# Optimization experiments

Measured on AMD Instinct MI355X. Metric: run time of the kernel, lower is better.

The kernel has to match this reference:

```python
import jax, jax.numpy as jnp
import numpy as np

DIM = 576
SCALE = DIM ** -0.5  # num_heads=1 -> head_dim = dim
EPS = 1e-5


def _layernorm(x, g, b):
    mu = jnp.mean(x, axis=-1, keepdims=True)
    var = jnp.mean(jnp.square(x - mu), axis=-1, keepdims=True)
    return (x - mu) * jax.lax.rsqrt(var + EPS) * g + b


def _cross(x, y, lnx_g, lnx_b, lny_g, lny_b, lnz_g, lnz_b, Wq, Wk, Wv, Wp, bp):
    # x, y: [B, N, C]; attends y (query) over x (key/value), residual from normed x
    xn = _layernorm(x, lnx_g, lnx_b)
    yn = _layernorm(y, lny_g, lny_b)
    q = jnp.einsum('bnd,od->bno', yn, Wq)
    k = jnp.einsum('bnd,od->bno', xn, Wk)
    v = jnp.einsum('bnd,od->bno', xn, Wv)
    attn = jax.nn.sigmoid(jnp.einsum('bqd,bkd->bqk', q, k) * SCALE)  # [B,N,N]
    o = jnp.einsum('bqk,bkd->bqd', attn, v)
    o = jnp.einsum('bnd,od->bno', o, Wp) + bp + xn
    return _layernorm(o, lnz_g, lnz_b)


def setup_inputs() -> dict:
    key = jax.random.key(0)
    ks = jax.random.split(key, 16)
    B, N, C = 8, 1024, DIM
    s = C ** -0.5
    inp = {
        'image_t': jax.random.normal(ks[0], (B, N, C), jnp.float32),
        'aolp_t': jax.random.normal(ks[1], (B, N, C), jnp.float32),
        'dolp_t': jax.random.normal(ks[2], (B, N, C), jnp.float32),
        # 6 Cross blocks, params stacked along axis 0
        'lnx_g': jnp.ones((6, C), jnp.float32),
        'lnx_b': jnp.zeros((6, C), jnp.float32),
        'lny_g': jnp.ones((6, C), jnp.float32),
        'lny_b': jnp.zeros((6, C), jnp.float32),
        'lnz_g': jnp.ones((6, C), jnp.float32),
        'lnz_b': jnp.zeros((6, C), jnp.float32),
        'Wq': jax.random.normal(ks[3], (6, C, C), jnp.float32) * s,
        'Wk': jax.random.normal(ks[4], (6, C, C), jnp.float32) * s,
        'Wv': jax.random.normal(ks[5], (6, C, C), jnp.float32) * s,
        'Wp': jax.random.normal(ks[6], (6, C, C), jnp.float32) * s,
        'bp': jnp.zeros((6, C), jnp.float32),
        'Wf': jax.random.normal(ks[7], (C, 6 * C), jnp.float32) * (6 * C) ** -0.5,
        'bf': jnp.zeros((C,), jnp.float32),
    }
    return inp


def reference(image_t, aolp_t, dolp_t, lnx_g, lnx_b, lny_g, lny_b, lnz_g, lnz_b,
              Wq, Wk, Wv, Wp, bp, Wf, bf):
    # pair order matches Fusion_T: (img,aolp),(img,dolp),(aolp,img),(aolp,dolp),(dolp,img),(dolp,aolp)
    xs = jnp.stack([image_t, image_t, aolp_t, aolp_t, dolp_t, dolp_t])  # [6,B,N,C]
    ys = jnp.stack([aolp_t, dolp_t, image_t, dolp_t, image_t, aolp_t])
    outs = jax.vmap(_cross)(xs, ys, lnx_g, lnx_b, lny_g, lny_b, lnz_g, lnz_b,
                            Wq, Wk, Wv, Wp, bp)  # [6,B,N,C]
    B, N, C = image_t.shape
    concat = jnp.transpose(outs, (1, 2, 0, 3)).reshape(B, N, 6 * C)
    fused = jnp.einsum('bnd,od->bno', concat, Wf) + bf
    return jax.nn.gelu(fused, approximate=False)
```

## Files before the change

### kernel.cpp

```cpp
#include <hip/hip_runtime.h>
#include <math.h>

#define LN_EPS 1e-5f

typedef short s8v __attribute__((ext_vector_type(8)));
typedef float f4v __attribute__((ext_vector_type(4)));

__device__ __forceinline__ short f2bf(float x) {
  union { float f; unsigned u; } v; v.f = x;
  const unsigned r = v.u + 0x7fffu + ((v.u >> 16) & 1u);
  return (short)(r >> 16);
}
__device__ __forceinline__ float bf2f(short s) {
  union { unsigned u; float f; } v;
  v.u = ((unsigned)(unsigned short)s) << 16;
  return v.f;
}

__device__ __forceinline__ void gld16(const void* g, void* l) {
  __builtin_amdgcn_global_load_lds(
      (const __attribute__((address_space(1))) void*)g,
      (__attribute__((address_space(3))) void*)l, 16, 0, 0);
}

enum { EP_SPLIT = 0, EP_SPLIT_T, EP_SIG, EP_RES, EP_BIAS, EP_ACC, EP_ACCGELU };

template <int EP, int WC>
__global__ __launch_bounds__(128 * WC) void gemmk(
    const short* __restrict__ Ah, const short* __restrict__ Al,
    const short* __restrict__ Bh, const short* __restrict__ Bl,
    short* __restrict__ Ch, short* __restrict__ Cl, float* __restrict__ Cf,
    const float* __restrict__ bias, const short* __restrict__ resH,
    const short* __restrict__ resL, float* __restrict__ out2, int pnCnt,
    int pmCnt, int lda, int ldb, int ldc, int K, long sA, long sB, long sC,
    float scale) {
  constexpr int BM = 128, BN = 64 * WC, T = 128 * WC;
  constexpr int RA = (BM * 128) / (T * 16);
  constexpr int RB = (BN * 128) / (T * 16);
  __shared__ short lds[(2 * BM + 2 * BN) * 64];
  short* AsH = lds;
  short* AsL = lds + BM * 64;
  short* BsH = lds + 2 * BM * 64;
  short* BsL = lds + 2 * BM * 64 + BN * 64;

  const int tid = threadIdx.x;
  const int lane = tid & 63;
  const int wave = tid >> 6;
  const int wr = wave / WC;
  const int wc = wave % WC;
  const int half = lane >> 4;
  const int l15 = lane & 15;

  const int chunk = gridDim.x >> 3;
  const int l = ((int)blockIdx.x & 7) * chunk + ((int)blockIdx.x >> 3);
  const int pn = l % pnCnt;
  const int t1 = l / pnCnt;
  const int pm = t1 % pmCnt;
  const long zb = t1 / pmCnt;
  const int bm = pm * BM;
  const int bn = pn * BN;

  Ah += zb * sA; Al += zb * sA;
  Bh += zb * sB; Bl += zb * sB;

  f4v acc[4][4];
#pragma unroll
  for (int i = 0; i < 4; ++i)
#pragma unroll
    for (int j = 0; j < 4; ++j)
#pragma unroll
      for (int r = 0; r < 4; ++r) acc[i][j][r] = 0.f;

  for (int k0 = 0; k0 < K; k0 += 64) {
    __syncthreads();
#pragma unroll
    for (int t = 0; t < RA; ++t) {
      const int off = (t * T + tid) * 16;
      const int row = off >> 7;
      const int ke = ((((off >> 4) & 7) ^ (row & 7)) << 3);
      const long ga = (long)(bm + row) * lda + k0 + ke;
      gld16(Ah + ga, (char*)AsH + off);
      gld16(Al + ga, (char*)AsL + off);
    }
#pragma unroll
    for (int t = 0; t < RB; ++t) {
      const int off = (t * T + tid) * 16;
      const int row = off >> 7;
      const int ke = ((((off >> 4) & 7) ^ (row & 7)) << 3);
      const long gb = (long)(bn + row) * ldb + k0 + ke;
      gld16(Bh + gb, (char*)BsH + off);
      gld16(Bl + gb, (char*)BsL + off);
    }
    __syncthreads();

#pragma unroll
    for (int s = 0; s < 2; ++s) {
      s8v ah[4], al[4], bh[4], bl[4];
#pragma unroll
      for (int i = 0; i < 4; ++i) {
        const int r = wr * 64 + i * 16 + l15;
        const int ad = r * 64 + ((((s << 2) + half) ^ (r & 7)) << 3);
        ah[i] = *(const s8v*)&AsH[ad];
        al[i] = *(const s8v*)&AsL[ad];
      }
#pragma unroll
      for (int j = 0; j < 4; ++j) {
        const int c = wc * 64 + j * 16 + l15;
        const int bd = c * 64 + ((((s << 2) + half) ^ (c & 7)) << 3);
        bh[j] = *(const s8v*)&BsH[bd];
        bl[j] = *(const s8v*)&BsL[bd];
      }
#pragma unroll
      for (int i = 0; i < 4; ++i)
#pragma unroll
        for (int j = 0; j < 4; ++j) {
          acc[i][j] = __builtin_amdgcn_mfma_f32_16x16x32_bf16(ah[i], bh[j],
                                                              acc[i][j], 0, 0, 0);
          acc[i][j] = __builtin_amdgcn_mfma_f32_16x16x32_bf16(ah[i], bl[j],
                                                              acc[i][j], 0, 0, 0);
          acc[i][j] = __builtin_amdgcn_mfma_f32_16x16x32_bf16(al[i], bh[j],
                                                              acc[i][j], 0, 0, 0);
        }
    }
  }

#pragma unroll
  for (int i = 0; i < 4; ++i) {
#pragma unroll
    for (int r = 0; r < 4; ++r) {
      const int row = bm + wr * 64 + i * 16 + half * 4 + r;
#pragma unroll
      for (int j = 0; j < 4; ++j) {
        const int col = bn + wc * 64 + j * 16 + l15;
        float x = acc[i][j][r];
        if (EP == EP_SPLIT) {
          const long idx = zb * sC + (long)row * ldc + col;
          const short h = f2bf(x);
          Ch[idx] = h;
          Cl[idx] = f2bf(x - bf2f(h));
        } else if (EP == EP_SPLIT_T) {
          const long idx = ((long)(row >> 10) * 576 + col) * 1024 + (row & 1023);
          const short h = f2bf(x);
          Ch[idx] = h;
          Cl[idx] = f2bf(x - bf2f(h));
        } else if (EP == EP_SIG) {
          x = 1.f / (1.f + expf(-x * scale));
          const long idx = zb * sC + (long)row * ldc + col;
          const short h = f2bf(x);
          Ch[idx] = h;
          Cl[idx] = f2bf(x - bf2f(h));
        } else if (EP == EP_RES) {
          const long idx = (long)row * ldc + col;
          Cf[idx] = x + bias[col] + bf2f(resH[idx]) + bf2f(resL[idx]);
        } else if (EP == EP_BIAS) {
          const long idx = (long)row * ldc + col;
          Cf[idx] = x + bias[col];
        } else if (EP == EP_ACC) {
          const long idx = (long)row * ldc + col;
          Cf[idx] += x;
        } else if (EP == EP_ACCGELU) {
          const long idx = (long)row * ldc + col;
          const float sum = Cf[idx] + x;
          out2[idx] = 0.5f * sum * (1.f + erff(sum * 0.70710678118654752f));
        }
      }
    }
  }
}

__global__ __launch_bounds__(576) void ln576(const float* __restrict__ x,
                                             const float* __restrict__ g,
                                             const float* __restrict__ b,
                                             short* __restrict__ oh,
                                             short* __restrict__ ol) {
  __shared__ float red[2][9];
  __shared__ float mu_s, rs_s;
  const long row = blockIdx.x;
  const int t = threadIdx.x;
  const float v = x[row * 576 + t];
  float s = v, s2 = v * v;
#pragma unroll
  for (int off = 32; off > 0; off >>= 1) {
    s += __shfl_xor(s, off);
    s2 += __shfl_xor(s2, off);
  }
  if ((t & 63) == 0) {
    red[0][t >> 6] = s;
    red[1][t >> 6] = s2;
  }
  __syncthreads();
  if (t == 0) {
    float a = 0.f, a2 = 0.f;
#pragma unroll
    for (int i = 0; i < 9; ++i) {
      a += red[0][i];
      a2 += red[1][i];
    }
    const float mu = a * (1.f / 576.f);
    mu_s = mu;
    rs_s = rsqrtf(a2 * (1.f / 576.f) - mu * mu + LN_EPS);
  }
  __syncthreads();
  const float y = (v - mu_s) * rs_s * g[t] + b[t];
  const short h = f2bf(y);
  oh[row * 576 + t] = h;
  ol[row * 576 + t] = f2bf(y - bf2f(h));
}

__global__ __launch_bounds__(256) void splitk(const float* __restrict__ in,
                                              short* __restrict__ oh,
                                              short* __restrict__ ol, long n) {
  long i = (long)blockIdx.x * blockDim.x + threadIdx.x;
  const long stride = (long)gridDim.x * blockDim.x;
  for (; i < n; i += stride) {
    const float x = in[i];
    const short h = f2bf(x);
    oh[i] = h;
    ol[i] = f2bf(x - bf2f(h));
  }
}

extern "C" void kernel_launch(void* const* d_in, const int* in_sizes, int n_in,
                              void* d_out, int out_size, void* d_ws,
                              size_t ws_size, hipStream_t stream) {
  const float* img = (const float*)d_in[0];
  const float* aolp = (const float*)d_in[1];
  const float* dolp = (const float*)d_in[2];
  const float* lnx_g = (const float*)d_in[3];
  const float* lnx_b = (const float*)d_in[4];
  const float* lny_g = (const float*)d_in[5];
  const float* lny_b = (const float*)d_in[6];
  const float* lnz_g = (const float*)d_in[7];
  const float* lnz_b = (const float*)d_in[8];
  const float* Wq = (const float*)d_in[9];
  const float* Wk = (const float*)d_in[10];
  const float* Wv = (const float*)d_in[11];
  const float* Wp = (const float*)d_in[12];
  const float* bp = (const float*)d_in[13];
  const float* Wf = (const float*)d_in[14];
  const float* bf = (const float*)d_in[15];
  float* out = (float*)d_out;

  const long S = 8L * 1024 * 576;
  const long W = 6L * 576 * 576;
  char* p = (char*)d_ws;
  auto alloc = [&](long bytes) {
    char* r = p;
    p += (bytes + 255) & ~255L;
    return r;
  };
  short* xn_h = (short*)alloc(S * 2);
  short* xn_l = (short*)alloc(S * 2);
  short* yn_h = (short*)alloc(S * 2);
  short* yn_l = (short*)alloc(S * 2);
  short* q_h = (short*)alloc(S * 2);
  short* q_l = (short*)alloc(S * 2);
  short* k_h = (short*)alloc(S * 2);
  short* k_l = (short*)alloc(S * 2);
  short* vt_h = (short*)alloc(S * 2);
  short* vt_l = (short*)alloc(S * 2);
  short* attn_h = (short*)alloc(8L * 1024 * 1024 * 2 * 2);
  short* attn_l = attn_h + 8L * 1024 * 1024;
  float* t_f32 = (float*)attn_h;
  float* fused = (float*)alloc(S * 4);
  short* wq_h = (short*)alloc(W * 2);
  short* wq_l = (short*)alloc(W * 2);
  short* wk_h = (short*)alloc(W * 2);
  short* wk_l = (short*)alloc(W * 2);
  short* wv_h = (short*)alloc(W * 2);
  short* wv_l = (short*)alloc(W * 2);
  short* wp_h = (short*)alloc(W * 2);
  short* wp_l = (short*)alloc(W * 2);
  short* wf_h = (short*)alloc(W * 2);
  short* wf_l = (short*)alloc(W * 2);

  splitk<<<1024, 256, 0, stream>>>(Wq, wq_h, wq_l, W);
  splitk<<<1024, 256, 0, stream>>>(Wk, wk_h, wk_l, W);
  splitk<<<1024, 256, 0, stream>>>(Wv, wv_h, wv_l, W);
  splitk<<<1024, 256, 0, stream>>>(Wp, wp_h, wp_l, W);
  splitk<<<1024, 256, 0, stream>>>(Wf, wf_h, wf_l, W);

  const float* src[3] = {img, aolp, dolp};
  const int xi[6] = {0, 0, 1, 1, 2, 2};
  const int yi[6] = {1, 2, 0, 2, 0, 1};
  const float scale = 1.f / 24.f;

  const int nProj = 9 * 64;
  const int nScore = 8 * 8 * 8;
  const int nAV = 9 * 8 * 8;

  for (int z = 0; z < 6; ++z) {
    const long wo = (long)z * 576 * 576;
    ln576<<<8192, 576, 0, stream>>>(src[xi[z]], lnx_g + z * 576,
                                    lnx_b + z * 576, xn_h, xn_l);
    ln576<<<8192, 576, 0, stream>>>(src[yi[z]], lny_g + z * 576,
                                    lny_b + z * 576, yn_h, yn_l);
    gemmk<EP_SPLIT, 1><<<nProj, 128, 0, stream>>>(
        yn_h, yn_l, wq_h + wo, wq_l + wo, q_h, q_l, nullptr, nullptr, nullptr,
        nullptr, nullptr, 9, 64, 576, 576, 576, 576, 0, 0, 0, 0.f);
    gemmk<EP_SPLIT, 1><<<nProj, 128, 0, stream>>>(
        xn_h, xn_l, wk_h + wo, wk_l + wo, k_h, k_l, nullptr, nullptr, nullptr,
        nullptr, nullptr, 9, 64, 576, 576, 576, 576, 0, 0, 0, 0.f);
    gemmk<EP_SPLIT_T, 1><<<nProj, 128, 0, stream>>>(
        xn_h, xn_l, wv_h + wo, wv_l + wo, vt_h, vt_l, nullptr, nullptr, nullptr,
        nullptr, nullptr, 9, 64, 576, 576, 0, 576, 0, 0, 0, 0.f);
    gemmk<EP_SIG, 2><<<nScore, 256, 0, stream>>>(
        q_h, q_l, k_h, k_l, attn_h, attn_l, nullptr, nullptr, nullptr, nullptr,
        nullptr, 8, 8, 576, 576, 1024, 576, 1024L * 576, 1024L * 576,
        1024L * 1024, scale);
    gemmk<EP_SPLIT, 1><<<nAV, 128, 0, stream>>>(
        attn_h, attn_l, vt_h, vt_l, yn_h, yn_l, nullptr, nullptr, nullptr,
        nullptr, nullptr, 9, 8, 1024, 1024, 576, 1024, 1024L * 1024,
        576L * 1024, 1024L * 576, 0.f);
    gemmk<EP_RES, 1><<<nProj, 128, 0, stream>>>(
        yn_h, yn_l, wp_h + wo, wp_l + wo, nullptr, nullptr, t_f32, bp + z * 576,
        xn_h, xn_l, nullptr, 9, 64, 576, 576, 576, 576, 0, 0, 0, 0.f);
    ln576<<<8192, 576, 0, stream>>>(t_f32, lnz_g + z * 576, lnz_b + z * 576,
                                    q_h, q_l);
    if (z == 0)
      gemmk<EP_BIAS, 1><<<nProj, 128, 0, stream>>>(
          q_h, q_l, wf_h + z * 576, wf_l + z * 576, nullptr, nullptr, fused, bf,
          nullptr, nullptr, nullptr, 9, 64, 576, 3456, 576, 576, 0, 0, 0, 0.f);
    else if (z < 5)
      gemmk<EP_ACC, 1><<<nProj, 128, 0, stream>>>(
          q_h, q_l, wf_h + z * 576, wf_l + z * 576, nullptr, nullptr, fused,
          nullptr, nullptr, nullptr, nullptr, 9, 64, 576, 3456, 576, 576, 0, 0,
          0, 0.f);
    else
      gemmk<EP_ACCGELU, 1><<<nProj, 128, 0, stream>>>(
          q_h, q_l, wf_h + z * 576, wf_l + z * 576, nullptr, nullptr, fused,
          nullptr, nullptr, nullptr, out, 9, 64, 576, 3456, 576, 576, 0, 0, 0,
          0.f);
  }
}
```

Measured before the change: 1.787 ms.

## Batch the six cross-attention blocks into grouped launches and fuse the final projection

Adds a group dimension (zz) to the GEMM and layernorm kernels so up to six cross blocks run inside one launch each, with the group size chosen from the available workspace. The per-block final-projection accumulation is replaced by writing every normalized block output into a concatenated [8192,3456] buffer, followed by a single K=3456 GEMM with a fused bias+GELU epilogue. This removes many small launches, removes the serial dependency between blocks, and fills the GPU better, but it needs much more workspace (per-group attention and activation buffers) and falls back to the old path when memory is short.

Measured after the change: 1.908 ms. +6.8%, slower.

```diff
diff --git a/kernel.cpp b/kernel.cpp
--- a/kernel.cpp
+++ b/kernel.cpp
@@ -23,7 +23,8 @@
       (__attribute__((address_space(3))) void*)l, 16, 0, 0);
 }
 
-enum { EP_SPLIT = 0, EP_SPLIT_T, EP_SIG, EP_RES, EP_BIAS, EP_ACC, EP_ACCGELU };
+enum { EP_SPLIT = 0, EP_SPLIT_T, EP_SIG, EP_RES, EP_BIAS, EP_ACC, EP_ACCGELU,
+       EP_GELUB };
 
 template <int EP, int WC>
 __global__ __launch_bounds__(128 * WC) void gemmk(
@@ -32,8 +33,8 @@
     short* __restrict__ Ch, short* __restrict__ Cl, float* __restrict__ Cf,
     const float* __restrict__ bias, const short* __restrict__ resH,
     const short* __restrict__ resL, float* __restrict__ out2, int pnCnt,
-    int pmCnt, int lda, int ldb, int ldc, int K, long sA, long sB, long sC,
-    float scale) {
+    int pmCnt, int bCnt, int lda, int ldb, int ldc, int K, long sA, long sB,
+    long sC, long sAz, long sBz, long sCz, long sRz, int biasZ, float scale) {
   constexpr int BM = 128, BN = 64 * WC, T = 128 * WC;
   constexpr int RA = (BM * 128) / (T * 16);
   constexpr int RB = (BN * 128) / (T * 16);
@@ -56,12 +57,17 @@
   const int pn = l % pnCnt;
   const int t1 = l / pnCnt;
   const int pm = t1 % pmCnt;
-  const long zb = t1 / pmCnt;
+  const int t2 = t1 / pmCnt;
+  const int bz = t2 % bCnt;
+  const int zz = t2 / bCnt;
   const int bm = pm * BM;
   const int bn = pn * BN;
 
-  Ah += zb * sA; Al += zb * sA;
-  Bh += zb * sB; Bl += zb * sB;
+  Ah += bz * sA + zz * sAz;
+  Al += bz * sA + zz * sAz;
+  Bh += bz * sB + zz * sBz;
+  Bl += bz * sB + zz * sBz;
+  const long cOff = bz * sC + (long)zz * sCz;
 
   f4v acc[4][4];
 #pragma unroll
@@ -134,33 +140,40 @@
         const int col = bn + wc * 64 + j * 16 + l15;
         float x = acc[i][j][r];
         if (EP == EP_SPLIT) {
-          const long idx = zb * sC + (long)row * ldc + col;
+          const long idx = cOff + (long)row * ldc + col;
           const short h = f2bf(x);
           Ch[idx] = h;
           Cl[idx] = f2bf(x - bf2f(h));
         } else if (EP == EP_SPLIT_T) {
-          const long idx = ((long)(row >> 10) * 576 + col) * 1024 + (row & 1023);
+          const long idx =
+              cOff + ((long)(row >> 10) * 576 + col) * 1024 + (row & 1023);
           const short h = f2bf(x);
           Ch[idx] = h;
           Cl[idx] = f2bf(x - bf2f(h));
         } else if (EP == EP_SIG) {
           x = 1.f / (1.f + expf(-x * scale));
-          const long idx = zb * sC + (long)row * ldc + col;
+          const long idx = cOff + (long)row * ldc + col;
           const short h = f2bf(x);
           Ch[idx] = h;
           Cl[idx] = f2bf(x - bf2f(h));
         } else if (EP == EP_RES) {
-          const long idx = (long)row * ldc + col;
-          Cf[idx] = x + bias[col] + bf2f(resH[idx]) + bf2f(resL[idx]);
+          const long idx = cOff + (long)row * ldc + col;
+          const long ridx = zz * sRz + (long)row * ldc + col;
+          Cf[idx] = x + bias[zz * biasZ + col] + bf2f(resH[ridx]) +
+                    bf2f(resL[ridx]);
         } else if (EP == EP_BIAS) {
-          const long idx = (long)row * ldc + col;
-          Cf[idx] = x + bias[col];
+          const long idx = cOff + (long)row * ldc + col;
+          Cf[idx] = x + bias[zz * biasZ + col];
         } else if (EP == EP_ACC) {
-          const long idx = (long)row * ldc + col;
+          const long idx = cOff + (long)row * ldc + col;
           Cf[idx] += x;
         } else if (EP == EP_ACCGELU) {
-          const long idx = (long)row * ldc + col;
+          const long idx = cOff + (long)row * ldc + col;
           const float sum = Cf[idx] + x;
+          out2[idx] = 0.5f * sum * (1.f + erff(sum * 0.70710678118654752f));
+        } else if (EP == EP_GELUB) {
+          const long idx = cOff + (long)row * ldc + col;
+          const float sum = x + bias[zz * biasZ + col];
           out2[idx] = 0.5f * sum * (1.f + erff(sum * 0.70710678118654752f));
         }
       }
@@ -168,16 +181,22 @@
   }
 }
 
-__global__ __launch_bounds__(576) void ln576(const float* __restrict__ x,
-                                             const float* __restrict__ g,
-                                             const float* __restrict__ b,
-                                             short* __restrict__ oh,
-                                             short* __restrict__ ol) {
+struct LnSrc {
+  const float* p[6];
+};
+
+__global__ __launch_bounds__(576) void ln576b(LnSrc srcs,
+                                              const float* __restrict__ g,
+                                              const float* __restrict__ b,
+                                              short* __restrict__ oh,
+                                              short* __restrict__ ol, long oz,
+                                              int ldo) {
   __shared__ float red[2][9];
   __shared__ float mu_s, rs_s;
-  const long row = blockIdx.x;
+  const int zz = blockIdx.x >> 13;
+  const long row = blockIdx.x & 8191;
   const int t = threadIdx.x;
-  const float v = x[row * 576 + t];
+  const float v = srcs.p[zz][row * 576 + t];
   float s = v, s2 = v * v;
 #pragma unroll
   for (int off = 32; off > 0; off >>= 1) {
@@ -201,10 +220,11 @@
     rs_s = rsqrtf(a2 * (1.f / 576.f) - mu * mu + LN_EPS);
   }
   __syncthreads();
-  const float y = (v - mu_s) * rs_s * g[t] + b[t];
+  const float y = (v - mu_s) * rs_s * g[zz * 576 + t] + b[zz * 576 + t];
   const short h = f2bf(y);
-  oh[row * 576 + t] = h;
-  ol[row * 576 + t] = f2bf(y - bf2f(h));
+  const long idx = zz * oz + row * ldo + t;
+  oh[idx] = h;
+  ol[idx] = f2bf(y - bf2f(h));
 }
 
 __global__ __launch_bounds__(256) void splitk(const float* __restrict__ in,
@@ -243,36 +263,44 @@
 
   const long S = 8L * 1024 * 576;
   const long W = 6L * 576 * 576;
+  const long AT = 16L * 1024 * 1024;
+
+  const long fixed = 10 * (W * 2 + 256) + 4 * (8192L * 3456 * 2 + 256);
+  const long perz = 10 * (S * 2 + 256) + (AT * 2 + 256);
+  int G = 1;
+  bool mega = true;
+  if ((long)ws_size >= fixed + 6 * perz) G = 6;
+  else if ((long)ws_size >= fixed + 3 * perz) G = 3;
+  else if ((long)ws_size >= fixed + 2 * perz) G = 2;
+  else if ((long)ws_size >= fixed + 1 * perz) G = 1;
+  else { G = 1; mega = false; }
+
   char* p = (char*)d_ws;
   auto alloc = [&](long bytes) {
     char* r = p;
     p += (bytes + 255) & ~255L;
     return r;
   };
-  short* xn_h = (short*)alloc(S * 2);
-  short* xn_l = (short*)alloc(S * 2);
-  short* yn_h = (short*)alloc(S * 2);
-  short* yn_l = (short*)alloc(S * 2);
-  short* q_h = (short*)alloc(S * 2);
-  short* q_l = (short*)alloc(S * 2);
-  short* k_h = (short*)alloc(S * 2);
-  short* k_l = (short*)alloc(S * 2);
-  short* vt_h = (short*)alloc(S * 2);
-  short* vt_l = (short*)alloc(S * 2);
-  short* attn_h = (short*)alloc(8L * 1024 * 1024 * 2 * 2);
-  short* attn_l = attn_h + 8L * 1024 * 1024;
-  float* t_f32 = (float*)attn_h;
-  float* fused = (float*)alloc(S * 4);
-  short* wq_h = (short*)alloc(W * 2);
-  short* wq_l = (short*)alloc(W * 2);
-  short* wk_h = (short*)alloc(W * 2);
-  short* wk_l = (short*)alloc(W * 2);
-  short* wv_h = (short*)alloc(W * 2);
-  short* wv_l = (short*)alloc(W * 2);
-  short* wp_h = (short*)alloc(W * 2);
-  short* wp_l = (short*)alloc(W * 2);
-  short* wf_h = (short*)alloc(W * 2);
-  short* wf_l = (short*)alloc(W * 2);
+  short* wq_h = (short*)alloc(W * 2); short* wq_l = (short*)alloc(W * 2);
+  short* wk_h = (short*)alloc(W * 2); short* wk_l = (short*)alloc(W * 2);
+  short* wv_h = (short*)alloc(W * 2); short* wv_l = (short*)alloc(W * 2);
+  short* wp_h = (short*)alloc(W * 2); short* wp_l = (short*)alloc(W * 2);
+  short* wf_h = (short*)alloc(W * 2); short* wf_l = (short*)alloc(W * 2);
+  short* zn_h = nullptr; short* zn_l = nullptr; float* fused = nullptr;
+  if (mega) {
+    zn_h = (short*)alloc(8192L * 3456 * 2);
+    zn_l = (short*)alloc(8192L * 3456 * 2);
+  }
+  short* xn_h = (short*)alloc(G * S * 2); short* xn_l = (short*)alloc(G * S * 2);
+  short* yn_h = (short*)alloc(G * S * 2); short* yn_l = (short*)alloc(G * S * 2);
+  short* q_h = (short*)alloc(G * S * 2);  short* q_l = (short*)alloc(G * S * 2);
+  short* k_h = (short*)alloc(G * S * 2);  short* k_l = (short*)alloc(G * S * 2);
+  short* vt_h = (short*)alloc(G * S * 2); short* vt_l = (short*)alloc(G * S * 2);
+  short* attnA = (short*)alloc(G * AT * 2);
+  short* attn_h = attnA;
+  short* attn_l = attnA + 8388608;
+  float* t_f32 = (float*)attnA;
+  if (!mega) fused = (float*)alloc(S * 4);
 
   splitk<<<1024, 256, 0, stream>>>(Wq, wq_h, wq_l, W);
   splitk<<<1024, 256, 0, stream>>>(Wk, wk_h, wk_l, W);
@@ -284,52 +312,72 @@
   const int xi[6] = {0, 0, 1, 1, 2, 2};
   const int yi[6] = {1, 2, 0, 2, 0, 1};
   const float scale = 1.f / 24.f;
-
-  const int nProj = 9 * 64;
-  const int nScore = 8 * 8 * 8;
-  const int nAV = 9 * 8 * 8;
-
-  for (int z = 0; z < 6; ++z) {
-    const long wo = (long)z * 576 * 576;
-    ln576<<<8192, 576, 0, stream>>>(src[xi[z]], lnx_g + z * 576,
-                                    lnx_b + z * 576, xn_h, xn_l);
-    ln576<<<8192, 576, 0, stream>>>(src[yi[z]], lny_g + z * 576,
-                                    lny_b + z * 576, yn_h, yn_l);
-    gemmk<EP_SPLIT, 1><<<nProj, 128, 0, stream>>>(
-        yn_h, yn_l, wq_h + wo, wq_l + wo, q_h, q_l, nullptr, nullptr, nullptr,
-        nullptr, nullptr, 9, 64, 576, 576, 576, 576, 0, 0, 0, 0.f);
-    gemmk<EP_SPLIT, 1><<<nProj, 128, 0, stream>>>(
-        xn_h, xn_l, wk_h + wo, wk_l + wo, k_h, k_l, nullptr, nullptr, nullptr,
-        nullptr, nullptr, 9, 64, 576, 576, 576, 576, 0, 0, 0, 0.f);
-    gemmk<EP_SPLIT_T, 1><<<nProj, 128, 0, stream>>>(
-        xn_h, xn_l, wv_h + wo, wv_l + wo, vt_h, vt_l, nullptr, nullptr, nullptr,
-        nullptr, nullptr, 9, 64, 576, 576, 0, 576, 0, 0, 0, 0.f);
-    gemmk<EP_SIG, 2><<<nScore, 256, 0, stream>>>(
+  const long WZ = 576L * 576;
+  const long TZ = 8388608;
+
+  for (int g0 = 0; g0 < 6; g0 += G) {
+    LnSrc sx, sy, st;
+    for (int zz = 0; zz < G; ++zz) {
+      sx.p[zz] = src[xi[g0 + zz]];
+      sy.p[zz] = src[yi[g0 + zz]];
+      st.p[zz] = t_f32 + zz * TZ;
+    }
+    ln576b<<<8192 * G, 576, 0, stream>>>(sx, lnx_g + g0 * 576, lnx_b + g0 * 576,
+                                         xn_h, xn_l, S, 576);
+    ln576b<<<8192 * G, 576, 0, stream>>>(sy, lny_g + g0 * 576, lny_b + g0 * 576,
+                                         yn_h, yn_l, S, 576);
+    gemmk<EP_SPLIT, 1><<<576 * G, 128, 0, stream>>>(
+        yn_h, yn_l, wq_h + g0 * WZ, wq_l + g0 * WZ, q_h, q_l, nullptr, nullptr,
+        nullptr, nullptr, nullptr, 9, 64, 1, 576, 576, 576, 576, 0, 0, 0, S, WZ,
+        S, 0, 0, 0.f);
+    gemmk<EP_SPLIT, 1><<<576 * G, 128, 0, stream>>>(
+        xn_h, xn_l, wk_h + g0 * WZ, wk_l + g0 * WZ, k_h, k_l, nullptr, nullptr,
+        nullptr, nullptr, nullptr, 9, 64, 1, 576, 576, 576, 576, 0, 0, 0, S, WZ,
+        S, 0, 0, 0.f);
+    gemmk<EP_SPLIT_T, 1><<<576 * G, 128, 0, stream>>>(
+        xn_h, xn_l, wv_h + g0 * WZ, wv_l + g0 * WZ, vt_h, vt_l, nullptr,
+        nullptr, nullptr, nullptr, nullptr, 9, 64, 1, 576, 576, 0, 576, 0, 0, 0,
+        S, WZ, S, 0, 0, 0.f);
+    gemmk<EP_SIG, 2><<<512 * G, 256, 0, stream>>>(
         q_h, q_l, k_h, k_l, attn_h, attn_l, nullptr, nullptr, nullptr, nullptr,
-        nullptr, 8, 8, 576, 576, 1024, 576, 1024L * 576, 1024L * 576,
-        1024L * 1024, scale);
-    gemmk<EP_SPLIT, 1><<<nAV, 128, 0, stream>>>(
+        nullptr, 8, 8, 8, 576, 576, 1024, 576, 1024L * 576, 1024L * 576,
+        1024L * 1024, S, S, AT, 0, 0, scale);
+    gemmk<EP_SPLIT, 1><<<576 * G, 128, 0, stream>>>(
         attn_h, attn_l, vt_h, vt_l, yn_h, yn_l, nullptr, nullptr, nullptr,
-        nullptr, nullptr, 9, 8, 1024, 1024, 576, 1024, 1024L * 1024,
-        576L * 1024, 1024L * 576, 0.f);
-    gemmk<EP_RES, 1><<<nProj, 128, 0, stream>>>(
-        yn_h, yn_l, wp_h + wo, wp_l + wo, nullptr, nullptr, t_f32, bp + z * 576,
-        xn_h, xn_l, nullptr, 9, 64, 576, 576, 576, 576, 0, 0, 0, 0.f);
-    ln576<<<8192, 576, 0, stream>>>(t_f32, lnz_g + z * 576, lnz_b + z * 576,
-                                    q_h, q_l);
-    if (z == 0)
-      gemmk<EP_BIAS, 1><<<nProj, 128, 0, stream>>>(
-          q_h, q_l, wf_h + z * 576, wf_l + z * 576, nullptr, nullptr, fused, bf,
-          nullptr, nullptr, nullptr, 9, 64, 576, 3456, 576, 576, 0, 0, 0, 0.f);
-    else if (z < 5)
-      gemmk<EP_ACC, 1><<<nProj, 128, 0, stream>>>(
-          q_h, q_l, wf_h + z * 576, wf_l + z * 576, nullptr, nullptr, fused,
-          nullptr, nullptr, nullptr, nullptr, 9, 64, 576, 3456, 576, 576, 0, 0,
-          0, 0.f);
-    else
-      gemmk<EP_ACCGELU, 1><<<nProj, 128, 0, stream>>>(
-          q_h, q_l, wf_h + z * 576, wf_l + z * 576, nullptr, nullptr, fused,
-          nullptr, nullptr, nullptr, out, 9, 64, 576, 3456, 576, 576, 0, 0, 0,
-          0.f);
-  }
-}
+        nullptr, nullptr, 9, 8, 8, 1024, 1024, 576, 1024, 1024L * 1024,
+        576L * 1024, 1024L * 576, AT, S, S, 0, 0, 0.f);
+    gemmk<EP_RES, 1><<<576 * G, 128, 0, stream>>>(
+        yn_h, yn_l, wp_h + g0 * WZ, wp_l + g0 * WZ, nullptr, nullptr, t_f32,
+        bp + g0 * 576, xn_h, xn_l, nullptr, 9, 64, 1, 576, 576, 576, 576, 0, 0,
+        0, S, WZ, TZ, S, 576, 0.f);
+    if (mega) {
+      ln576b<<<8192 * G, 576, 0, stream>>>(st, lnz_g + g0 * 576,
+                                           lnz_b + g0 * 576, zn_h + g0 * 576,
+                                           zn_l + g0 * 576, 576L, 3456);
+    } else {
+      const int z = g0;
+      ln576b<<<8192, 576, 0, stream>>>(st, lnz_g + z * 576, lnz_b + z * 576,
+                                       q_h, q_l, 0, 576);
+      if (z == 0)
+        gemmk<EP_BIAS, 1><<<576, 128, 0, stream>>>(
+            q_h, q_l, wf_h + z * 576, wf_l + z * 576, nullptr, nullptr, fused,
+            bf, nullptr, nullptr, nullptr, 9, 64, 1, 576, 3456, 576, 576, 0, 0,
+            0, 0, 0, 0, 0, 0, 0.f);
+      else if (z < 5)
+        gemmk<EP_ACC, 1><<<576, 128, 0, stream>>>(
+            q_h, q_l, wf_h + z * 576, wf_l + z * 576, nullptr, nullptr, fused,
+            nullptr, nullptr, nullptr, nullptr, 9, 64, 1, 576, 3456, 576, 576,
+            0, 0, 0, 0, 0, 0, 0, 0, 0.f);
+      else
+        gemmk<EP_ACCGELU, 1><<<576, 128, 0, stream>>>(
+            q_h, q_l, wf_h + z * 576, wf_l + z * 576, nullptr, nullptr, fused,
+            nullptr, nullptr, nullptr, out, 9, 64, 1, 576, 3456, 576, 576, 0, 0,
+            0, 0, 0, 0, 0, 0, 0.f);
+    }
+  }
+  if (mega) {
+    gemmk<EP_GELUB, 1><<<576, 128, 0, stream>>>(
+        zn_h, zn_l, wf_h, wf_l, nullptr, nullptr, nullptr, bf, nullptr, nullptr,
+        out, 9, 64, 1, 3456, 3456, 576, 3456, 0, 0, 0, 0, 0, 0, 0, 0, 0.f);
+  }
+}
```
